# Kernel optimization log

Measured on AMD Instinct MI355X. Metric: run time of the kernel, lower is better.

## Reference

```python
import math
import jax, jax.numpy as jnp
import numpy as np

B, IMG, P, D, DEPTH, NH, HD = 8, 384, 16, 768, 12, 12, 64
NREG, NS, NF = 4, 5, 16            # registers, special tokens (1 cls + 4 reg), rope freqs
HP = IMG // P                      # 24 patches per side
NPATCH = HP * HP                   # 576
ROPE_DIM = 2 * NF                  # 32
SCALE = HD ** -0.5


def setup_inputs() -> dict:
    key = jax.random.key(0)
    ks = jax.random.split(key, 12)
    s = 0.02
    rn = lambda k, shape: (jax.random.normal(k, shape, jnp.float32) * s)
    L, DF = DEPTH, 4 * D
    inp = {
        "pixel_values": jax.random.normal(ks[0], (B, 3, IMG, IMG), jnp.float32),
        "conv_w": rn(ks[1], (D, 3, P, P)),
        "conv_b": jnp.zeros((D,), jnp.float32),
        "cls_token": rn(ks[2], (1, 1, D)),
        "storage_tokens": rn(ks[3], (1, NREG, D)),
        "periods": jnp.exp(jnp.linspace(0.0, math.log(100.0), NF)).astype(jnp.float32),
        "ln1_s": jnp.ones((L, D), jnp.float32),
        "ln1_b": jnp.zeros((L, D), jnp.float32),
        "qkv_w": rn(ks[4], (L, 3 * D, D)),
        "qkv_b": rn(ks[5], (L, 3 * D)),
        "bias_mask": jnp.zeros((L, 3 * D), jnp.float32),  # buffer init zeros -> bias nulled
        "proj_w": rn(ks[6], (L, D, D)),
        "proj_b": jnp.zeros((L, D), jnp.float32),
        "ls1": jnp.ones((L, D), jnp.float32),
        "ln2_s": jnp.ones((L, D), jnp.float32),
        "ln2_b": jnp.zeros((L, D), jnp.float32),
        "fc1_w": rn(ks[7], (L, DF, D)),
        "fc1_b": jnp.zeros((L, DF), jnp.float32),
        "fc2_w": rn(ks[8], (L, D, DF)),
        "fc2_b": jnp.zeros((L, D), jnp.float32),
        "ls2": jnp.ones((L, D), jnp.float32),
        "lnf_s": jnp.ones((D,), jnp.float32),
        "lnf_b": jnp.zeros((D,), jnp.float32),
    }
    return inp


def _ln(x, s, b):
    mu = x.mean(-1, keepdims=True)
    var = ((x - mu) ** 2).mean(-1, keepdims=True)
    return (x - mu) / jnp.sqrt(var + 1e-6) * s + b


def _rot(x, cos, sin):
    # x: [b, h, n_patch, 2*NF]; cos/sin: [n_patch, NF]; interleaved even/odd rotation
    even, odd = x[..., 0::2], x[..., 1::2]
    return jnp.stack([even * cos - odd * sin, even * sin + odd * cos], axis=-1).reshape(x.shape)


def _forward(pixel_values, conv_w, conv_b, cls_token, storage_tokens, periods,
             ln1_s, ln1_b, qkv_w, qkv_b, bias_mask, proj_w, proj_b, ls1,
             ln2_s, ln2_b, fc1_w, fc1_b, fc2_w, fc2_b, ls2, lnf_s, lnf_b):
    b = pixel_values.shape[0]
    # Patch embed: stride == kernel conv as reshape + einsum
    xp = pixel_values.reshape(b, 3, HP, P, HP, P)
    tok = jnp.einsum('bchpwq,dcpq->bhwd', xp, conv_w) + conv_b       # [b,HP,HP,D]
    tok = tok.reshape(b, NPATCH, D)
    x = jnp.concatenate([jnp.broadcast_to(cls_token, (b, 1, D)),
                         jnp.broadcast_to(storage_tokens, (b, NREG, D)), tok], axis=1)
    n = x.shape[1]

    # RoPE tables (periods buffer; freqs = 2*pi / periods)
    freqs = (2.0 * math.pi) / periods                                 # [NF]
    pos = jnp.arange(HP, dtype=jnp.float32)
    gy, gx = jnp.meshgrid(pos, pos, indexing='ij')
    ax = gx.reshape(-1, 1) * freqs                                    # [NPATCH, NF]
    ay = gy.reshape(-1, 1) * freqs
    cos_x, sin_x = jnp.cos(ax), jnp.sin(ax)
    cos_y, sin_y = jnp.cos(ay), jnp.sin(ay)

    def blk(h, p):
        (l1s, l1b, qw, qb, bm, pw, pb, g1, l2s, l2b, f1w, f1b, f2w, f2b, g2) = p
        h1 = _ln(h, l1s, l1b)
        qkv = h1 @ qw.T + qb * bm                                     # bias nulled by mask
        qkv = qkv.reshape(b, n, 3, NH, HD).transpose(2, 0, 3, 1, 4)   # [3,b,NH,n,HD]
        q, k, v = qkv[0], qkv[1], qkv[2]
        # rotary on patch tokens; rope_total == HD so the whole head is rotated
        qp, kp = q[:, :, NS:], k[:, :, NS:]
        qp = jnp.concatenate([_rot(qp[..., :ROPE_DIM], cos_x, sin_x),
                              _rot(qp[..., ROPE_DIM:], cos_y, sin_y)], axis=-1)
        kp = jnp.concatenate([_rot(kp[..., :ROPE_DIM], cos_x, sin_x),
                              _rot(kp[..., ROPE_DIM:], cos_y, sin_y)], axis=-1)
        q = jnp.concatenate([q[:, :, :NS], qp], axis=2)
        k = jnp.concatenate([k[:, :, :NS], kp], axis=2)
        attn = jax.nn.softmax(jnp.einsum('bhqd,bhkd->bhqk', q, k) * SCALE, axis=-1)
        o = jnp.einsum('bhqk,bhkd->bhqd', attn, v).transpose(0, 2, 1, 3).reshape(b, n, D)
        h = h + g1 * (o @ pw.T + pb)
        h2 = _ln(h, l2s, l2b)
        m = jax.nn.gelu(h2 @ f1w.T + f1b, approximate=False) @ f2w.T + f2b
        h = h + g2 * m
        return h, None

    params = (ln1_s, ln1_b, qkv_w, qkv_b, bias_mask, proj_w, proj_b, ls1,
              ln2_s, ln2_b, fc1_w, fc1_b, fc2_w, fc2_b, ls2)
    x, _ = jax.lax.scan(blk, x, params)
    return _ln(x, lnf_s, lnf_b)


def reference(pixel_values, conv_w, conv_b, cls_token, storage_tokens, periods,
              ln1_s, ln1_b, qkv_w, qkv_b, bias_mask, proj_w, proj_b, ls1,
              ln2_s, ln2_b, fc1_w, fc1_b, fc2_w, fc2_b, ls2, lnf_s, lnf_b):
    return _forward(pixel_values, conv_w, conv_b, cls_token, storage_tokens, periods,
                    ln1_s, ln1_b, qkv_w, qkv_b, bias_mask, proj_w, proj_b, ls1,
                    ln2_s, ln2_b, fc1_w, fc1_b, fc2_w, fc2_b, ls2, lnf_s, lnf_b)
```

## Files before the change

### kernel.cpp

```cpp
#include <hip/hip_runtime.h>
#include <math.h>

typedef unsigned short u16;
typedef __attribute__((ext_vector_type(8))) short bf8;
typedef __attribute__((ext_vector_type(4))) float f4;

#define DEV static __device__ __forceinline__

DEV u16 f2b(float f){
  unsigned u = __builtin_bit_cast(unsigned, f);
  u += 0x7fffu + ((u >> 16) & 1u);
  return (u16)(u >> 16);
}
DEV float b2f(u16 h){
  unsigned u = ((unsigned)h) << 16;
  return __builtin_bit_cast(float, u);
}

#define BATCH  8
#define NTOK   581
#define NPAD   640
#define DIM    768
#define DFF    3072
#define NHEAD  12
#define HDIM   64
#define NLAYER 12
#define MTOK   (BATCH*NTOK)
#define MPAD2  4736
#define MCONV  (BATCH*576)
#define ATTN_SCALE 0.125f
#define BHEADS (BATCH*NHEAD)
#define QSZ    ((long long)BHEADS*NPAD*HDIM)

enum { EPI_CONV=0, EPI_QKV, EPI_PROJ, EPI_GELU, EPI_FC2 };

DEV int xcdswz(int lin, int n){
  int q = n >> 3, r = n & 7;
  int x = lin & 7, o = lin >> 3;
  return (x < r ? x*(q+1) : r*(q+1) + (x - r)*q) + o;
}

template<int EPI, int BM, int BN, int NWAVE>
__global__ __launch_bounds__(NWAVE*64) void gemmRS(
    const u16* __restrict__ A, int lda,
    const u16* __restrict__ B, int ldb, int K,
    const float* __restrict__ bias,
    const float* __restrict__ aux,
    float* __restrict__ Cf,
    u16* __restrict__ Cb)
{
  constexpr int NT = NWAVE * 64;
  constexpr int SR = NT / 4;
  constexpr int AL = BM / SR, BL = BN / SR;
  constexpr int WROWS = (NWAVE == 8) ? 4 : 2;
  constexpr int WCOLS = NWAVE / WROWS;
  constexpr int TR = BM / WROWS, TC = BN / WCOLS;
  constexpr int MR = TR / 16, NR = TC / 16;
  const int gx = gridDim.x;
  const int lin = blockIdx.y * gx + blockIdx.x;
  const int tix = xcdswz(lin, gx * gridDim.y);
  const int bm = (tix / gx) * BM, bn = (tix % gx) * BN;
  __shared__ __attribute__((aligned(16))) u16 As[2][BM][40];
  __shared__ __attribute__((aligned(16))) u16 Bs[2][BN][40];
  const int tid  = threadIdx.x;
  const int lane = tid & 63, wid = tid >> 6;
  const int wr = wid % WROWS, wc = wid / WROWS;
  const int srow = tid >> 2, scol = (tid & 3) * 8;
  const u16* gA[AL]; const u16* gB[BL];
  #pragma unroll
  for (int i = 0; i < AL; ++i) gA[i] = A + (long long)(bm + i*SR + srow) * lda + scol;
  #pragma unroll
  for (int i = 0; i < BL; ++i) gB[i] = B + (long long)(bn + i*SR + srow) * ldb + scol;
  const int frow = lane & 15, quad = lane >> 4, fk = quad * 8;

  f4 acc[MR][NR] = {};
  const int T = K >> 5;

  bf8 xA[AL], xB[BL], yA[AL], yB[BL];
  auto loadX = [&](int kt){
    #pragma unroll
    for (int i = 0; i < AL; ++i) xA[i] = *(const bf8*)(gA[i] + kt*32);
    #pragma unroll
    for (int i = 0; i < BL; ++i) xB[i] = *(const bf8*)(gB[i] + kt*32);
  };
  auto loadY = [&](int kt){
    #pragma unroll
    for (int i = 0; i < AL; ++i) yA[i] = *(const bf8*)(gA[i] + kt*32);
    #pragma unroll
    for (int i = 0; i < BL; ++i) yB[i] = *(const bf8*)(gB[i] + kt*32);
  };
  auto storeX = [&](int buf){
    #pragma unroll
    for (int i = 0; i < AL; ++i) *(bf8*)&As[buf][i*SR + srow][scol] = xA[i];
    #pragma unroll
    for (int i = 0; i < BL; ++i) *(bf8*)&Bs[buf][i*SR + srow][scol] = xB[i];
  };
  auto storeY = [&](int buf){
    #pragma unroll
    for (int i = 0; i < AL; ++i) *(bf8*)&As[buf][i*SR + srow][scol] = yA[i];
    #pragma unroll
    for (int i = 0; i < BL; ++i) *(bf8*)&Bs[buf][i*SR + srow][scol] = yB[i];
  };
  auto compute = [&](int buf){
    bf8 af[MR], bf[NR];
    #pragma unroll
    for (int m = 0; m < MR; ++m)
      af[m] = *(const bf8*)&As[buf][wr*TR + m*16 + frow][fk];
    #pragma unroll
    for (int n = 0; n < NR; ++n)
      bf[n] = *(const bf8*)&Bs[buf][wc*TC + n*16 + frow][fk];
    #pragma unroll
    for (int m = 0; m < MR; ++m)
    #pragma unroll
    for (int n = 0; n < NR; ++n)
      acc[m][n] = __builtin_amdgcn_mfma_f32_16x16x32_bf16(af[m], bf[n], acc[m][n], 0, 0, 0);
  };

  loadX(0); loadY(1);
  storeX(0);
  __syncthreads();

  for (int t = 0; t < T; t += 2){
    if (t + 2 < T) loadX(t + 2);
    storeY(1);
    compute(0);
    __syncthreads();
    if (t + 3 < T) loadY(t + 3);
    if (t + 2 < T) storeX(0);
    compute(1);
    __syncthreads();
  }

  #pragma unroll
  for (int mi = 0; mi < MR; ++mi)
  #pragma unroll
  for (int ni = 0; ni < NR; ++ni){
    f4 v = acc[mi][ni];
    int col = bn + wc*TC + ni*16 + frow;
    int r0  = bm + wr*TR + mi*16 + quad*4;
    #pragma unroll
    for (int j = 0; j < 4; ++j){
      int m = r0 + j;
      float val = v[j];
      if constexpr (EPI == EPI_CONV){
        int b = m / 576, p = m % 576;
        Cf[((long long)b*NTOK + 5 + p)*DIM + col] = val + bias[col];
      } else if constexpr (EPI == EPI_QKV){
        if (m < MTOK){
          int b = m / NTOK, tt = m % NTOK;
          int which = col / DIM, rem = col % DIM;
          int h = rem / HDIM, hd = rem % HDIM;
          float x = val + bias[col];
          if (which == 0) x *= ATTN_SCALE;
          if (which < 2 && tt >= 5){
            float po = __shfl_xor(x, 1);
            int p = tt - 5;
            int f = (hd & 31) >> 1;
            int pc = (hd < 32) ? (p % 24) : (p / 24);
            float c = aux[pc*16 + f];
            float s = aux[384 + pc*16 + f];
            x = (hd & 1) ? (po*s + x*c) : (x*c - po*s);
          }
          long long bh = (long long)(b*NHEAD + h);
          if (which == 2)
            Cb[2*QSZ + (bh*HDIM + hd)*NPAD + tt] = f2b(x);
          else
            Cb[(long long)which*QSZ + (bh*NPAD + tt)*HDIM + hd] = f2b(x);
        }
      } else if constexpr (EPI == EPI_PROJ || EPI == EPI_FC2){
        if (m < MTOK)
          Cf[(long long)m*DIM + col] += aux[col] * (val + bias[col]);
      } else if constexpr (EPI == EPI_GELU){
        float x = val + bias[col];
        float g = 0.5f * x * (1.0f + erff(x * 0.70710678118f));
        Cb[(long long)m*DFF + col] = f2b(g);
      }
    }
  }
}

__global__ __launch_bounds__(256) void flash_k(
    const u16* __restrict__ Q, const u16* __restrict__ K,
    const u16* __restrict__ VT, u16* __restrict__ obuf)
{
  const int lid = blockIdx.x;
  const int xcd = lid & 7, slot = lid >> 3;
  const int bh = xcd * 12 + slot / 5;
  const int qb = slot % 5;
  const int b = bh / NHEAD, h = bh % NHEAD;
  const int tid = threadIdx.x, lane = tid & 63, w = tid >> 6;
  const int frow = lane & 15, quad = lane >> 4;
  __shared__ u16 P[4][2][16][80];
  const u16* Qb = Q  + (long long)bh * NPAD * HDIM;
  const u16* Kb = K  + (long long)bh * NPAD * HDIM;
  const u16* Vb = VT + (long long)bh * HDIM * NPAD;
  bf8 qa0[2], qa1[2];
  #pragma unroll
  for (int bd = 0; bd < 2; ++bd){
    const u16* qr = &Qb[(qb*128 + bd*64 + w*16 + frow)*HDIM + quad*8];
    qa0[bd] = *(const bf8*)qr;
    qa1[bd] = *(const bf8*)(qr + 32);
  }
  f4 o[2][4] = {};
  float m[2][4], l[2][4];
  #pragma unroll
  for (int bd = 0; bd < 2; ++bd)
  #pragma unroll
  for (int j = 0; j < 4; ++j){ m[bd][j] = -1e30f; l[bd][j] = 0.0f; }

  bf8 kb0[4], kb1[4];
  #pragma unroll
  for (int n = 0; n < 4; ++n){
    const u16* kr = &Kb[(n*16 + frow)*HDIM + quad*8];
    kb0[n] = *(const bf8*)kr;
    kb1[n] = *(const bf8*)(kr + 32);
  }

  for (int kt = 0; kt < NPAD/64; ++kt){
    bf8 vb0[4], vb1[4];
    #pragma unroll
    for (int n = 0; n < 4; ++n){
      const u16* vr = &Vb[(n*16 + frow)*NPAD + kt*64 + quad*8];
      vb0[n] = *(const bf8*)vr;
      vb1[n] = *(const bf8*)(vr + 32);
    }
    f4 s[2][4];
    __builtin_amdgcn_s_setprio(1);
    #pragma unroll
    for (int n = 0; n < 4; ++n)
    #pragma unroll
    for (int bd = 0; bd < 2; ++bd){
      f4 z = {};
      z        = __builtin_amdgcn_mfma_f32_16x16x32_bf16(qa0[bd], kb0[n], z, 0, 0, 0);
      s[bd][n] = __builtin_amdgcn_mfma_f32_16x16x32_bf16(qa1[bd], kb1[n], z, 0, 0, 0);
    }
    __builtin_amdgcn_s_setprio(0);
    if (kt + 1 < NPAD/64){
      #pragma unroll
      for (int n = 0; n < 4; ++n){
        const u16* kr = &Kb[((kt+1)*64 + n*16 + frow)*HDIM + quad*8];
        kb0[n] = *(const bf8*)kr;
        kb1[n] = *(const bf8*)(kr + 32);
      }
    }
    if (kt == NPAD/64 - 1){
      #pragma unroll
      for (int n = 0; n < 4; ++n){
        int kcol = kt*64 + n*16 + frow;
        if (kcol >= NTOK){
          #pragma unroll
          for (int bd = 0; bd < 2; ++bd)
            s[bd][n][0] = s[bd][n][1] = s[bd][n][2] = s[bd][n][3] = -1e30f;
        }
      }
    }
    #pragma unroll
    for (int bd = 0; bd < 2; ++bd){
      float tv[4];
      int need = 0;
      #pragma unroll
      for (int j = 0; j < 4; ++j){
        float v = fmaxf(fmaxf(s[bd][0][j], s[bd][1][j]), fmaxf(s[bd][2][j], s[bd][3][j]));
        v = fmaxf(v, __shfl_xor(v, 1));  v = fmaxf(v, __shfl_xor(v, 2));
        v = fmaxf(v, __shfl_xor(v, 4));  v = fmaxf(v, __shfl_xor(v, 8));
        tv[j] = v;
        need |= (v > m[bd][j] + 8.0f) ? 1 : 0;
      }
      if (__any(need)){
        #pragma unroll
        for (int j = 0; j < 4; ++j){
          float mn = fmaxf(m[bd][j], tv[j]);
          float sc = __expf(m[bd][j] - mn);
          m[bd][j] = mn;
          l[bd][j] *= sc;
          #pragma unroll
          for (int n = 0; n < 4; ++n) o[bd][n][j] *= sc;
        }
      }
      float ts[4] = {0.f, 0.f, 0.f, 0.f};
      #pragma unroll
      for (int n = 0; n < 4; ++n){
        #pragma unroll
        for (int j = 0; j < 4; ++j){
          float p = __expf(s[bd][n][j] - m[bd][j]);
          ts[j] += p;
          P[w][bd][quad*4 + j][n*16 + frow] = f2b(p);
        }
      }
      #pragma unroll
      for (int j = 0; j < 4; ++j){
        float v = ts[j];
        v += __shfl_xor(v, 1); v += __shfl_xor(v, 2);
        v += __shfl_xor(v, 4); v += __shfl_xor(v, 8);
        l[bd][j] += v;
      }
      bf8 pa0 = *(const bf8*)&P[w][bd][frow][quad*8];
      bf8 pa1 = *(const bf8*)&P[w][bd][frow][quad*8 + 32];
      __builtin_amdgcn_s_setprio(1);
      #pragma unroll
      for (int n = 0; n < 4; ++n){
        o[bd][n] = __builtin_amdgcn_mfma_f32_16x16x32_bf16(pa0, vb0[n], o[bd][n], 0, 0, 0);
        o[bd][n] = __builtin_amdgcn_mfma_f32_16x16x32_bf16(pa1, vb1[n], o[bd][n], 0, 0, 0);
      }
      __builtin_amdgcn_s_setprio(0);
    }
  }
  #pragma unroll
  for (int bd = 0; bd < 2; ++bd)
  #pragma unroll
  for (int j = 0; j < 4; ++j){
    int t = qb*128 + bd*64 + w*16 + quad*4 + j;
    if (t < NTOK){
      float inv = 1.0f / l[bd][j];
      #pragma unroll
      for (int n = 0; n < 4; ++n)
        obuf[((long long)b*NTOK + t)*DIM + h*HDIM + n*16 + frow] = f2b(o[bd][n][j] * inv);
    }
  }
}

template<int F32OUT>
__global__ __launch_bounds__(256) void ln_k(const float* __restrict__ x,
    const float* __restrict__ s, const float* __restrict__ b,
    u16* __restrict__ ob, float* __restrict__ of)
{
  const long long row = blockIdx.x;
  const float* xr = x + row * DIM;
  const int t = threadIdx.x;
  float v0 = xr[t], v1 = xr[t + 256], v2 = xr[t + 512];
  float sum = v0 + v1 + v2;
  #pragma unroll
  for (int o = 32; o; o >>= 1) sum += __shfl_down(sum, o);
  __shared__ float r1[4], r2[4];
  const int lane = t & 63, w = t >> 6;
  if (lane == 0) r1[w] = sum;
  __syncthreads();
  float mu = (r1[0] + r1[1] + r1[2] + r1[3]) * (1.0f / DIM);
  float d0 = v0 - mu, d1 = v1 - mu, d2 = v2 - mu;
  float vs = d0*d0 + d1*d1 + d2*d2;
  #pragma unroll
  for (int o = 32; o; o >>= 1) vs += __shfl_down(vs, o);
  if (lane == 0) r2[w] = vs;
  __syncthreads();
  float inv = 1.0f / sqrtf((r2[0] + r2[1] + r2[2] + r2[3]) * (1.0f / DIM) + 1e-6f);
  if constexpr (F32OUT){
    float* orow = of + row * DIM;
    orow[t]       = d0 * inv * s[t]       + b[t];
    orow[t + 256] = d1 * inv * s[t + 256] + b[t + 256];
    orow[t + 512] = d2 * inv * s[t + 512] + b[t + 512];
  } else {
    u16* orow = ob + row * DIM;
    orow[t]       = f2b(d0 * inv * s[t]       + b[t]);
    orow[t + 256] = f2b(d1 * inv * s[t + 256] + b[t + 256]);
    orow[t + 512] = f2b(d2 * inv * s[t + 512] + b[t + 512]);
  }
}

__global__ void ropetab_k(const float* __restrict__ periods, float* __restrict__ tab)
{
  int idx = blockIdx.x * blockDim.x + threadIdx.x;
  if (idx >= 24 * 16) return;
  int c = idx >> 4, f = idx & 15;
  float fr = 6.283185307179586f / periods[f];
  float a = (float)c * fr;
  tab[idx]       = cosf(a);
  tab[384 + idx] = sinf(a);
}

__global__ void initx_k(float* __restrict__ x, const float* __restrict__ cls,
                        const float* __restrict__ stor)
{
  int idx = blockIdx.x * blockDim.x + threadIdx.x;
  if (idx >= BATCH * 5 * DIM) return;
  int d = idx % DIM; int t = (idx / DIM) % 5; int b = idx / (5 * DIM);
  x[((long long)b * NTOK + t) * DIM + d] = (t == 0) ? cls[d] : stor[(t - 1) * DIM + d];
}

__global__ void patch_k(const float* __restrict__ px, u16* __restrict__ Ap)
{
  int idx = blockIdx.x * blockDim.x + threadIdx.x;
  if (idx >= MCONV * DIM) return;
  int k = idx % DIM, m = idx / DIM;
  int b = m / 576, r = m % 576, hp = r / 24, wp = r % 24;
  int c = k / 256, rem = k % 256, p = rem / 16, q = rem % 16;
  float v = px[((((long long)b * 3 + c) * 384) + hp * 16 + p) * 384 + wp * 16 + q];
  Ap[idx] = f2b(v);
}

__global__ void cvt_k(const float* __restrict__ src, u16* __restrict__ dst, long long n)
{
  long long i = (long long)blockIdx.x * blockDim.x + threadIdx.x;
  long long stride = (long long)gridDim.x * blockDim.x;
  for (; i < n; i += stride) dst[i] = f2b(src[i]);
}

__global__ void biaseff_k(const float* __restrict__ qb, const float* __restrict__ bm,
                          float* __restrict__ out, int n)
{
  int i = blockIdx.x * blockDim.x + threadIdx.x;
  if (i < n) out[i] = qb[i] * bm[i];
}

extern "C" void kernel_launch(void* const* d_in, const int* in_sizes, int n_in,
                              void* d_out, int out_size, void* d_ws, size_t ws_size,
                              hipStream_t stream)
{
  const float* pixel   = (const float*)d_in[0];
  const float* conv_w  = (const float*)d_in[1];
  const float* conv_b  = (const float*)d_in[2];
  const float* cls     = (const float*)d_in[3];
  const float* stor    = (const float*)d_in[4];
  const float* periods = (const float*)d_in[5];
  const float* ln1s    = (const float*)d_in[6];
  const float* ln1b    = (const float*)d_in[7];
  const float* qkvw    = (const float*)d_in[8];
  const float* qkvb    = (const float*)d_in[9];
  const float* bmask   = (const float*)d_in[10];
  const float* projw   = (const float*)d_in[11];
  const float* projb   = (const float*)d_in[12];
  const float* ls1     = (const float*)d_in[13];
  const float* ln2s    = (const float*)d_in[14];
  const float* ln2b    = (const float*)d_in[15];
  const float* fc1w    = (const float*)d_in[16];
  const float* fc1b    = (const float*)d_in[17];
  const float* fc2w    = (const float*)d_in[18];
  const float* fc2b    = (const float*)d_in[19];
  const float* ls2     = (const float*)d_in[20];
  const float* lnfs    = (const float*)d_in[21];
  const float* lnfb    = (const float*)d_in[22];

  char* wsp = (char*)d_ws;
  auto alloc = [&](long long bytes) -> char* {
    char* p = wsp; wsp += (bytes + 255) & ~255LL; return p;
  };
  u16*   wqkv  = (u16*)  alloc((long long)NLAYER*2304*768*2);
  u16*   wproj = (u16*)  alloc((long long)NLAYER*768*768*2);
  u16*   wfc1  = (u16*)  alloc((long long)NLAYER*3072*768*2);
  u16*   wfc2  = (u16*)  alloc((long long)NLAYER*768*3072*2);
  u16*   wconv = (u16*)  alloc((long long)768*768*2);
  float* beff  = (float*)alloc((long long)NLAYER*2304*4);
  float* x     = (float*)alloc((long long)MPAD2*DIM*4);
  u16*   h     = (u16*)  alloc((long long)MPAD2*DIM*2);
  u16*   obuf  = (u16*)  alloc((long long)MPAD2*DIM*2);
  u16*   mlp   = (u16*)  alloc((long long)MPAD2*DFF*2);
  u16*   Ap    = (u16*)  alloc((long long)MCONV*DIM*2);
  u16*   Q     = (u16*)  alloc(QSZ*2*3);
  u16*   Kb    = Q + QSZ;
  u16*   VT    = Q + 2*QSZ;
  float* tab   = (float*)alloc((long long)2*24*16*4);
  if ((size_t)(wsp - (char*)d_ws) > ws_size) return;

  auto cvt = [&](const float* src, u16* dst, long long n){
    long long nb = (n + 255) / 256; if (nb > 4096) nb = 4096;
    cvt_k<<<(int)nb, 256, 0, stream>>>(src, dst, n);
  };
  cvt(qkvw,  wqkv,  (long long)NLAYER*2304*768);
  cvt(projw, wproj, (long long)NLAYER*768*768);
  cvt(fc1w,  wfc1,  (long long)NLAYER*3072*768);
  cvt(fc2w,  wfc2,  (long long)NLAYER*768*3072);
  cvt(conv_w, wconv, (long long)768*768);
  biaseff_k<<<(NLAYER*2304 + 255)/256, 256, 0, stream>>>(qkvb, bmask, beff, NLAYER*2304);
  ropetab_k<<<2, 256, 0, stream>>>(periods, tab);
  hipMemsetAsync(Q, 0, (size_t)QSZ*2*3, stream);

  patch_k<<<(MCONV*DIM + 255)/256, 256, 0, stream>>>(pixel, Ap);
  initx_k<<<(BATCH*5*DIM + 255)/256, 256, 0, stream>>>(x, cls, stor);
  gemmRS<EPI_CONV,64,64,4><<<dim3(DIM/64, MCONV/64), 256, 0, stream>>>(
      Ap, DIM, wconv, DIM, DIM, conv_b, nullptr, x, nullptr);

  for (int l = 0; l < NLAYER; ++l){
    ln_k<0><<<MTOK, 256, 0, stream>>>(x, ln1s + l*DIM, ln1b + l*DIM, h, nullptr);
    gemmRS<EPI_QKV,128,64,4><<<dim3(2304/64, MPAD2/128), 256, 0, stream>>>(
        h, DIM, wqkv + (long long)l*2304*768, DIM, DIM,
        beff + l*2304, tab, nullptr, Q);
    flash_k<<<dim3(480), 256, 0, stream>>>(Q, Kb, VT, obuf);
    gemmRS<EPI_PROJ,64,64,4><<<dim3(DIM/64, MPAD2/64), 256, 0, stream>>>(
        obuf, DIM, wproj + (long long)l*768*768, DIM, DIM,
        projb + l*DIM, ls1 + l*DIM, x, nullptr);
    ln_k<0><<<MTOK, 256, 0, stream>>>(x, ln2s + l*DIM, ln2b + l*DIM, h, nullptr);
    gemmRS<EPI_GELU,128,64,4><<<dim3(DFF/64, MPAD2/128), 256, 0, stream>>>(
        h, DIM, wfc1 + (long long)l*3072*768, DIM, DIM,
        fc1b + l*DFF, nullptr, nullptr, mlp);
    gemmRS<EPI_FC2,128,64,4><<<dim3(DIM/64, MPAD2/128), 256, 0, stream>>>(
        mlp, DFF, wfc2 + (long long)l*768*3072, DFF, DFF,
        fc2b + l*DIM, ls2 + l*DIM, x, nullptr);
  }
  ln_k<1><<<MTOK, 256, 0, stream>>>(x, lnfs, lnfb, nullptr, (float*)d_out);
}
```

Measured before the change: 3.141 ms.

## Add three-deep register prefetch pipeline to GEMM and retile FC2

Adds a DEPTH template parameter to the bf16 MFMA GEMM. DEPTH 3 keeps three k-tiles of global loads in flight through registers while still using two LDS buffers, and is applied to the QKV and FC1 GEMMs (K=768, T=24, a multiple of 6). The aim is to hide more global memory latency behind MFMA work. Separately, FC2 moves from 128x64 to 64x64 tiles, doubling its grid to improve occupancy and load balance. The deeper pipeline costs extra registers and assumes T is divisible by 6.

New measurement: 3.175 ms. About the same (+1.1%).

```diff
diff --git a/kernel.cpp b/kernel.cpp
--- a/kernel.cpp
+++ b/kernel.cpp
@@ -40,7 +40,7 @@
   return (x < r ? x*(q+1) : r*(q+1) + (x - r)*q) + o;
 }
 
-template<int EPI, int BM, int BN, int NWAVE>
+template<int EPI, int BM, int BN, int NWAVE, int DEPTH>
 __global__ __launch_bounds__(NWAVE*64) void gemmRS(
     const u16* __restrict__ A, int lda,
     const u16* __restrict__ B, int ldb, int K,
@@ -76,7 +76,7 @@
   f4 acc[MR][NR] = {};
   const int T = K >> 5;
 
-  bf8 xA[AL], xB[BL], yA[AL], yB[BL];
+  bf8 xA[AL], xB[BL], yA[AL], yB[BL], zA[AL], zB[BL];
   auto loadX = [&](int kt){
     #pragma unroll
     for (int i = 0; i < AL; ++i) xA[i] = *(const bf8*)(gA[i] + kt*32);
@@ -89,6 +89,12 @@
     #pragma unroll
     for (int i = 0; i < BL; ++i) yB[i] = *(const bf8*)(gB[i] + kt*32);
   };
+  auto loadZ = [&](int kt){
+    #pragma unroll
+    for (int i = 0; i < AL; ++i) zA[i] = *(const bf8*)(gA[i] + kt*32);
+    #pragma unroll
+    for (int i = 0; i < BL; ++i) zB[i] = *(const bf8*)(gB[i] + kt*32);
+  };
   auto storeX = [&](int buf){
     #pragma unroll
     for (int i = 0; i < AL; ++i) *(bf8*)&As[buf][i*SR + srow][scol] = xA[i];
@@ -100,6 +106,12 @@
     for (int i = 0; i < AL; ++i) *(bf8*)&As[buf][i*SR + srow][scol] = yA[i];
     #pragma unroll
     for (int i = 0; i < BL; ++i) *(bf8*)&Bs[buf][i*SR + srow][scol] = yB[i];
+  };
+  auto storeZ = [&](int buf){
+    #pragma unroll
+    for (int i = 0; i < AL; ++i) *(bf8*)&As[buf][i*SR + srow][scol] = zA[i];
+    #pragma unroll
+    for (int i = 0; i < BL; ++i) *(bf8*)&Bs[buf][i*SR + srow][scol] = zB[i];
   };
   auto compute = [&](int buf){
     bf8 af[MR], bf[NR];
@@ -116,19 +128,39 @@
       acc[m][n] = __builtin_amdgcn_mfma_f32_16x16x32_bf16(af[m], bf[n], acc[m][n], 0, 0, 0);
   };
 
-  loadX(0); loadY(1);
-  storeX(0);
-  __syncthreads();
-
-  for (int t = 0; t < T; t += 2){
-    if (t + 2 < T) loadX(t + 2);
-    storeY(1);
-    compute(0);
+  if constexpr (DEPTH == 3){
+    loadX(0); loadY(1); loadZ(2);
+    storeX(0);
     __syncthreads();
-    if (t + 3 < T) loadY(t + 3);
-    if (t + 2 < T) storeX(0);
-    compute(1);
+    for (int t = 0; t < T; t += 6){
+      loadX(t + 3);
+      storeY(1); compute(0); __syncthreads();
+      loadY(t + 4);
+      storeZ(0); compute(1); __syncthreads();
+      loadZ(t + 5);
+      storeX(1); compute(0); __syncthreads();
+      if (t + 6 < T) loadX(t + 6);
+      storeY(0); compute(1); __syncthreads();
+      if (t + 7 < T) loadY(t + 7);
+      storeZ(1); compute(0); __syncthreads();
+      if (t + 8 < T) loadZ(t + 8);
+      if (t + 6 < T) storeX(0);
+      compute(1); __syncthreads();
+    }
+  } else {
+    loadX(0); loadY(1);
+    storeX(0);
     __syncthreads();
+    for (int t = 0; t < T; t += 2){
+      if (t + 2 < T) loadX(t + 2);
+      storeY(1);
+      compute(0);
+      __syncthreads();
+      if (t + 3 < T) loadY(t + 3);
+      if (t + 2 < T) storeX(0);
+      compute(1);
+      __syncthreads();
+    }
   }
 
   #pragma unroll
@@ -465,23 +497,23 @@
 
   patch_k<<<(MCONV*DIM + 255)/256, 256, 0, stream>>>(pixel, Ap);
   initx_k<<<(BATCH*5*DIM + 255)/256, 256, 0, stream>>>(x, cls, stor);
-  gemmRS<EPI_CONV,64,64,4><<<dim3(DIM/64, MCONV/64), 256, 0, stream>>>(
+  gemmRS<EPI_CONV,64,64,4,2><<<dim3(DIM/64, MCONV/64), 256, 0, stream>>>(
       Ap, DIM, wconv, DIM, DIM, conv_b, nullptr, x, nullptr);
 
   for (int l = 0; l < NLAYER; ++l){
     ln_k<0><<<MTOK, 256, 0, stream>>>(x, ln1s + l*DIM, ln1b + l*DIM, h, nullptr);
-    gemmRS<EPI_QKV,128,64,4><<<dim3(2304/64, MPAD2/128), 256, 0, stream>>>(
+    gemmRS<EPI_QKV,128,64,4,3><<<dim3(2304/64, MPAD2/128), 256, 0, stream>>>(
         h, DIM, wqkv + (long long)l*2304*768, DIM, DIM,
         beff + l*2304, tab, nullptr, Q);
     flash_k<<<dim3(480), 256, 0, stream>>>(Q, Kb, VT, obuf);
-    gemmRS<EPI_PROJ,64,64,4><<<dim3(DIM/64, MPAD2/64), 256, 0, stream>>>(
+    gemmRS<EPI_PROJ,64,64,4,2><<<dim3(DIM/64, MPAD2/64), 256, 0, stream>>>(
         obuf, DIM, wproj + (long long)l*768*768, DIM, DIM,
         projb + l*DIM, ls1 + l*DIM, x, nullptr);
     ln_k<0><<<MTOK, 256, 0, stream>>>(x, ln2s + l*DIM, ln2b + l*DIM, h, nullptr);
-    gemmRS<EPI_GELU,128,64,4><<<dim3(DFF/64, MPAD2/128), 256, 0, stream>>>(
+    gemmRS<EPI_GELU,128,64,4,3><<<dim3(DFF/64, MPAD2/128), 256, 0, stream>>>(
         h, DIM, wfc1 + (long long)l*3072*768, DIM, DIM,
         fc1b + l*DFF, nullptr, nullptr, mlp);
-    gemmRS<EPI_FC2,128,64,4><<<dim3(DIM/64, MPAD2/128), 256, 0, stream>>>(
+    gemmRS<EPI_FC2,64,64,4,2><<<dim3(DIM/64, MPAD2/64), 256, 0, stream>>>(
         mlp, DFF, wfc2 + (long long)l*768*3072, DFF, DFF,
         fc2b + l*DIM, ls2 + l*DIM, x, nullptr);
   }
```
